# Performance work log

Measured on AMD Instinct MI355X. Metric: run time of the kernel, lower is better.

The kernel has to match this reference:

```python
import jax, jax.numpy as jnp
import numpy as np

BATCH, IN_DIM, UNITS = 2048, 512, 512


def setup_inputs() -> dict:
    key = jax.random.key(0)
    k1, k2 = jax.random.split(key)
    x = jax.random.normal(k1, (BATCH, IN_DIM), dtype=jnp.float32)
    # He-style init for W, shape (1, in_dim, units) as in build()
    W = jax.random.normal(k2, (1, IN_DIM, UNITS), dtype=jnp.float32) * np.float32(np.sqrt(2.0 / IN_DIM))
    bias = jnp.zeros((UNITS,), dtype=jnp.float32)
    return {"x": x, "W": W, "bias": bias}


def reference(x, W, bias):
    # nodal 'exponential': exp(x * w) - 1, broadcast (batch,in,1)*(1,in,units)
    z = jnp.exp(x[:, :, None] * W) - 1.0          # (batch, in, units)
    # pool 'maximum': reduce over input dim
    p = jnp.max(z, axis=1)                         # (batch, units)
    # bias add + activation 'tanh'
    return jnp.tanh(p + bias)
```

## Files before the change

### kernel.cpp

```cpp
#include <hip/hip_runtime.h>


#define BATCH 2048
#define INDIM 512
#define UNITS 512

#define KC 32
#define RB 16
#define NW 16

typedef float v2f __attribute__((ext_vector_type(2)));

__global__ __launch_bounds__(1024, 8) void maxexp_kernel(
    const float* __restrict__ x,
    const float* __restrict__ W,
    const float* __restrict__ bias,
    float* __restrict__ out)
{
    __shared__ float part[RB][NW][64];

    const int f   = blockIdx.x;
    const int bg  = (f & 7) * 16 + ((f >> 3) & 15);
    const int ut  = f >> 7;

    const int lane = threadIdx.x & 63;
    const int wv   = __builtin_amdgcn_readfirstlane(threadIdx.x >> 6);
    const int u    = ut * 64 + lane;
    const int k0   = wv * KC;
    const int b0   = bg * RB;

    v2f wp[KC / 2];
    {
        const float* wb = W + (size_t)k0 * UNITS + u;
#pragma unroll
        for (int j = 0; j < KC / 2; ++j) {
            v2f t;
            t.x = wb[(size_t)(2 * j)     * UNITS];
            t.y = wb[(size_t)(2 * j + 1) * UNITS];
            wp[j] = t;
        }
    }
#pragma unroll
    for (int j = 0; j < KC / 2; ++j) asm("" : "+v"(wp[j]));

    const float* xb = x + (size_t)b0 * INDIM + k0;

    float acc[RB];
#pragma unroll
    for (int t = 0; t < RB; ++t) {
        const v2f* xr = reinterpret_cast<const v2f*>(xb + (size_t)t * INDIM);
        float m0 = -3.4e38f, m1 = -3.4e38f;
#pragma unroll
        for (int j = 0; j < KC / 2; j += 2) {
            v2f p0, p1;
            asm("v_pk_mul_f32 %0, %1, %2" : "=v"(p0) : "s"(xr[j]),     "v"(wp[j]));
            asm("v_pk_mul_f32 %0, %1, %2" : "=v"(p1) : "s"(xr[j + 1]), "v"(wp[j + 1]));
            m0 = fmaxf(fmaxf(m0, p0.x), p0.y);
            m1 = fmaxf(fmaxf(m1, p1.x), p1.y);
        }
        acc[t] = fmaxf(m0, m1);
    }

#pragma unroll
    for (int t = 0; t < RB; ++t) part[t][wv][lane] = acc[t];
    __syncthreads();

    {
        const int t = wv;
        float m = -3.4e38f;
#pragma unroll
        for (int j = 0; j < NW; j += 2)
            m = fmaxf(fmaxf(m, part[t][j][lane]), part[t][j + 1][lane]);
        const float pp = __expf(m) - 1.0f + bias[u];
        const float e  = __expf(2.0f * pp);
        out[(size_t)(b0 + t) * UNITS + u] = 1.0f - 2.0f / (e + 1.0f);
    }
}

extern "C" void kernel_launch(void* const* d_in, const int* in_sizes, int n_in,
                              void* d_out, int out_size, void* d_ws, size_t ws_size,
                              hipStream_t stream) {
    const float* x    = (const float*)d_in[0];
    const float* W    = (const float*)d_in[1];
    const float* bias = (const float*)d_in[2];
    float* out = (float*)d_out;

    dim3 grid(BATCH / RB * (UNITS / 64));
    dim3 block(1024);
    maxexp_kernel<<<grid, block, 0, stream>>>(x, W, bias, out);
}
```

Baseline: 26.06 us.

## Stage x rows in LDS and halve rows per block

The change halves rows per block from 16 to 8, so there are twice as many blocks. Each block now stages its 8 input rows into shared memory with one coalesced float4 load per thread, where before each wave read them through scalar loads. Waves then read x from LDS as broadcast float4s into VGPRs for the packed multiplies. In exchange it adds an extra barrier and LDS traffic, doubles the number of W register loads across the grid, and leaves half the waves idle in the final reduction.

Measured after the change: 29.00 us. 11.3% more time.

```diff
diff --git a/kernel.cpp b/kernel.cpp
--- a/kernel.cpp
+++ b/kernel.cpp
@@ -6,7 +6,7 @@
 #define UNITS 512
 
 #define KC 32
-#define RB 16
+#define RB 8
 #define NW 16
 
 typedef float v2f __attribute__((ext_vector_type(2)));
@@ -17,17 +17,25 @@
     const float* __restrict__ bias,
     float* __restrict__ out)
 {
+    __shared__ float xs[RB][INDIM];
     __shared__ float part[RB][NW][64];
 
-    const int f   = blockIdx.x;
-    const int bg  = (f & 7) * 16 + ((f >> 3) & 15);
-    const int ut  = f >> 7;
+    const int f    = blockIdx.x;
+    const int band = (f & 7) * 32 + ((f >> 3) & 31);
+    const int ut   = f >> 8;
 
-    const int lane = threadIdx.x & 63;
-    const int wv   = __builtin_amdgcn_readfirstlane(threadIdx.x >> 6);
+    const int tid  = threadIdx.x;
+    const int lane = tid & 63;
+    const int wv   = __builtin_amdgcn_readfirstlane(tid >> 6);
     const int u    = ut * 64 + lane;
     const int k0   = wv * KC;
-    const int b0   = bg * RB;
+    const int b0   = band * RB;
+
+    {
+        const float4 v = *reinterpret_cast<const float4*>(
+            x + (size_t)b0 * INDIM + (size_t)tid * 4);
+        *reinterpret_cast<float4*>(&xs[0][0] + (size_t)tid * 4) = v;
+    }
 
     v2f wp[KC / 2];
     {
@@ -43,29 +51,29 @@
 #pragma unroll
     for (int j = 0; j < KC / 2; ++j) asm("" : "+v"(wp[j]));
 
-    const float* xb = x + (size_t)b0 * INDIM + k0;
+    __syncthreads();
 
-    float acc[RB];
 #pragma unroll
     for (int t = 0; t < RB; ++t) {
-        const v2f* xr = reinterpret_cast<const v2f*>(xb + (size_t)t * INDIM);
+        const float4* xq = reinterpret_cast<const float4*>(&xs[t][k0]);
         float m0 = -3.4e38f, m1 = -3.4e38f;
 #pragma unroll
-        for (int j = 0; j < KC / 2; j += 2) {
-            v2f p0, p1;
-            asm("v_pk_mul_f32 %0, %1, %2" : "=v"(p0) : "s"(xr[j]),     "v"(wp[j]));
-            asm("v_pk_mul_f32 %0, %1, %2" : "=v"(p1) : "s"(xr[j + 1]), "v"(wp[j + 1]));
+        for (int q4 = 0; q4 < KC / 4; ++q4) {
+            const float4 q = xq[q4];
+            v2f a0, a1, p0, p1;
+            a0.x = q.x; a0.y = q.y;
+            a1.x = q.z; a1.y = q.w;
+            asm("v_pk_mul_f32 %0, %1, %2" : "=v"(p0) : "v"(a0), "v"(wp[2 * q4]));
+            asm("v_pk_mul_f32 %0, %1, %2" : "=v"(p1) : "v"(a1), "v"(wp[2 * q4 + 1]));
             m0 = fmaxf(fmaxf(m0, p0.x), p0.y);
             m1 = fmaxf(fmaxf(m1, p1.x), p1.y);
         }
-        acc[t] = fmaxf(m0, m1);
+        part[t][wv][lane] = fmaxf(m0, m1);
     }
 
-#pragma unroll
-    for (int t = 0; t < RB; ++t) part[t][wv][lane] = acc[t];
     __syncthreads();
 
-    {
+    if (wv < RB) {
         const int t = wv;
         float m = -3.4e38f;
 #pragma unroll
```

## Convert inputs to packed fp16 and compute products and max in half precision

Applied to the files above, without the earlier changes.

Adds a pre-pass kernel that converts x and pair-interleaved W to packed fp16 in the workspace. The main kernel then uses v_pk_mul_f16 and v_pk_max_f16, which handle two products per instruction and fold the max into packed ops instead of scalar fmaxf chains. This halves the ALU work per element and shrinks memory traffic. In exchange it adds an extra kernel launch plus a conversion pass, and it loses accuracy because products and maxima are rounded to fp16 before the exp.

Result: slower. 33.97 us (+30.4%).

```diff
diff --git a/kernel.cpp b/kernel.cpp
--- a/kernel.cpp
+++ b/kernel.cpp
@@ -1,79 +1,97 @@
 #include <hip/hip_runtime.h>
+#include <hip/hip_fp16.h>
 
 
 #define BATCH 2048
 #define INDIM 512
 #define UNITS 512
 
-#define KC 32
+#define KP 16
 #define RB 16
 #define NW 16
 
-typedef float v2f __attribute__((ext_vector_type(2)));
+#define XPAIRS (BATCH * INDIM / 2)
+#define WPAIRS (INDIM / 2 * UNITS)
+
+__global__ __launch_bounds__(256) void cvt_kernel(
+    const float* __restrict__ x, const float* __restrict__ W,
+    unsigned int* __restrict__ xh, unsigned int* __restrict__ wph)
+{
+    const int t = blockIdx.x * 256 + threadIdx.x;
+    if (t < XPAIRS) {
+        const float2 v = reinterpret_cast<const float2*>(x)[t];
+        xh[t] = (unsigned)__half_as_ushort(__float2half_rn(v.x))
+              | ((unsigned)__half_as_ushort(__float2half_rn(v.y)) << 16);
+    } else if (t - XPAIRS < WPAIRS) {
+        const int t2 = t - XPAIRS;
+        const int kp = t2 >> 9, u = t2 & 511;
+        const float a = W[(size_t)(2 * kp) * UNITS + u];
+        const float b = W[(size_t)(2 * kp + 1) * UNITS + u];
+        wph[t2] = (unsigned)__half_as_ushort(__float2half_rn(a))
+                | ((unsigned)__half_as_ushort(__float2half_rn(b)) << 16);
+    }
+}
 
 __global__ __launch_bounds__(1024, 8) void maxexp_kernel(
-    const float* __restrict__ x,
-    const float* __restrict__ W,
+    const unsigned int* __restrict__ xh,
+    const unsigned int* __restrict__ wph,
     const float* __restrict__ bias,
     float* __restrict__ out)
 {
-    __shared__ float part[RB][NW][64];
+    __shared__ unsigned int part[RB][NW][64];
 
-    const int f   = blockIdx.x;
-    const int bg  = (f & 7) * 16 + ((f >> 3) & 15);
-    const int ut  = f >> 7;
+    const int f    = blockIdx.x;
+    const int bg   = (f & 7) * 16 + ((f >> 3) & 15);
+    const int ut   = f >> 7;
 
     const int lane = threadIdx.x & 63;
     const int wv   = __builtin_amdgcn_readfirstlane(threadIdx.x >> 6);
     const int u    = ut * 64 + lane;
-    const int k0   = wv * KC;
+    const int kp0  = wv * KP;
     const int b0   = bg * RB;
 
-    v2f wp[KC / 2];
+    unsigned int wp[KP];
     {
-        const float* wb = W + (size_t)k0 * UNITS + u;
+        const unsigned int* wb = wph + (size_t)kp0 * UNITS + u;
 #pragma unroll
-        for (int j = 0; j < KC / 2; ++j) {
-            v2f t;
-            t.x = wb[(size_t)(2 * j)     * UNITS];
-            t.y = wb[(size_t)(2 * j + 1) * UNITS];
-            wp[j] = t;
-        }
+        for (int j = 0; j < KP; ++j) wp[j] = wb[(size_t)j * UNITS];
     }
 #pragma unroll
-    for (int j = 0; j < KC / 2; ++j) asm("" : "+v"(wp[j]));
+    for (int j = 0; j < KP; ++j) asm("" : "+v"(wp[j]));
 
-    const float* xb = x + (size_t)b0 * INDIM + k0;
+    const unsigned int* xb = xh + (size_t)b0 * (INDIM / 2) + kp0;
 
-    float acc[RB];
 #pragma unroll
     for (int t = 0; t < RB; ++t) {
-        const v2f* xr = reinterpret_cast<const v2f*>(xb + (size_t)t * INDIM);
-        float m0 = -3.4e38f, m1 = -3.4e38f;
+        const unsigned int* xr = xb + (size_t)t * (INDIM / 2);
+        unsigned int mA = 0xFC00FC00u, mB = 0xFC00FC00u;
 #pragma unroll
-        for (int j = 0; j < KC / 2; j += 2) {
-            v2f p0, p1;
-            asm("v_pk_mul_f32 %0, %1, %2" : "=v"(p0) : "s"(xr[j]),     "v"(wp[j]));
-            asm("v_pk_mul_f32 %0, %1, %2" : "=v"(p1) : "s"(xr[j + 1]), "v"(wp[j + 1]));
-            m0 = fmaxf(fmaxf(m0, p0.x), p0.y);
-            m1 = fmaxf(fmaxf(m1, p1.x), p1.y);
+        for (int j = 0; j < KP; j += 2) {
+            unsigned int p0, p1;
+            asm("v_pk_mul_f16 %0, %1, %2" : "=v"(p0) : "s"(xr[j]),     "v"(wp[j]));
+            asm("v_pk_mul_f16 %0, %1, %2" : "=v"(p1) : "s"(xr[j + 1]), "v"(wp[j + 1]));
+            asm("v_pk_max_f16 %0, %0, %1" : "+v"(mA) : "v"(p0));
+            asm("v_pk_max_f16 %0, %0, %1" : "+v"(mB) : "v"(p1));
         }
-        acc[t] = fmaxf(m0, m1);
+        asm("v_pk_max_f16 %0, %0, %1" : "+v"(mA) : "v"(mB));
+        part[t][wv][lane] = mA;
     }
 
-#pragma unroll
-    for (int t = 0; t < RB; ++t) part[t][wv][lane] = acc[t];
     __syncthreads();
 
     {
-        const int t = wv;
-        float m = -3.4e38f;
+        unsigned int m = part[wv][0][lane];
 #pragma unroll
-        for (int j = 0; j < NW; j += 2)
-            m = fmaxf(fmaxf(m, part[t][j][lane]), part[t][j + 1][lane]);
-        const float pp = __expf(m) - 1.0f + bias[u];
+        for (int j = 1; j < NW; ++j) {
+            const unsigned int pj = part[wv][j][lane];
+            asm("v_pk_max_f16 %0, %0, %1" : "+v"(m) : "v"(pj));
+        }
+        const float lo = __half2float(__ushort_as_half((unsigned short)(m & 0xffffu)));
+        const float hi = __half2float(__ushort_as_half((unsigned short)(m >> 16)));
+        const float mm = fmaxf(lo, hi);
+        const float pp = __expf(mm) - 1.0f + bias[u];
         const float e  = __expf(2.0f * pp);
-        out[(size_t)(b0 + t) * UNITS + u] = 1.0f - 2.0f / (e + 1.0f);
+        out[(size_t)(b0 + wv) * UNITS + u] = 1.0f - 2.0f / (e + 1.0f);
     }
 }
 
@@ -85,7 +103,13 @@
     const float* bias = (const float*)d_in[2];
     float* out = (float*)d_out;
 
+    unsigned int* xh  = (unsigned int*)d_ws;
+    unsigned int* wph = xh + XPAIRS;
+
+    const int cvt_blocks = (XPAIRS + WPAIRS + 255) / 256;
+    cvt_kernel<<<cvt_blocks, 256, 0, stream>>>(x, W, xh, wph);
+
     dim3 grid(BATCH / RB * (UNITS / 64));
     dim3 block(1024);
-    maxexp_kernel<<<grid, block, 0, stream>>>(x, W, bias, out);
+    maxexp_kernel<<<grid, block, 0, stream>>>(xh, wph, bias, out);
 }
```
